# Kernel tuning notes

Measured on AMD Instinct MI355X. Metric: run time of the kernel, lower is better.

## Reference

```python
import jax, jax.numpy as jnp
import numpy as np

B, N, C = 4, 8192, 256
H, L = 8, 64
HD = C // H            # head_dim = 32
NB = N // L            # num_blocks = 128
EG_HID = 16            # EDGE_GATE_HIDDEN_DIM


def setup_inputs() -> dict:
    key = jax.random.key(0)
    ks = jax.random.split(key, 10)
    x = jax.random.normal(ks[0], (B, N, C), dtype=jnp.float32)
    attn_mask = (jax.random.uniform(ks[1], (B, NB, L, L)) < 0.3).astype(jnp.float32)
    edge_feats = jax.random.normal(ks[2], (B, NB, L, L, 4), dtype=jnp.float32)
    # parameters
    qkv_w = jax.random.normal(ks[3], (3 * C, C), dtype=jnp.float32) * (C ** -0.5)
    qkv_b = jnp.zeros((3 * C,), dtype=jnp.float32)
    proj_w = jax.random.normal(ks[4], (C, C), dtype=jnp.float32) * (C ** -0.5)
    proj_b = jnp.zeros((C,), dtype=jnp.float32)
    eg_w1 = jax.random.normal(ks[5], (EG_HID, 4), dtype=jnp.float32) * 0.01
    eg_b1 = jnp.zeros((EG_HID,), dtype=jnp.float32)
    eg_w2 = jax.random.normal(ks[6], (H, EG_HID), dtype=jnp.float32) * 0.01
    eg_b2 = jnp.zeros((H,), dtype=jnp.float32)
    return {"x": x, "attn_mask": attn_mask, "edge_feats": edge_feats,
            "qkv_w": qkv_w, "qkv_b": qkv_b, "proj_w": proj_w, "proj_b": proj_b,
            "eg_w1": eg_w1, "eg_b1": eg_b1, "eg_w2": eg_w2, "eg_b2": eg_b2}


def reference(x, attn_mask, edge_feats, qkv_w, qkv_b, proj_w, proj_b,
              eg_w1, eg_b1, eg_w2, eg_b2):
    scale = HD ** -0.5
    xb = x.reshape(B, NB, L, C)                      # (B, nb, L, C)
    eye = jnp.eye(L, dtype=x.dtype)                  # (L, L)

    # ensure every query row attends to >= 1 key: OR-in diagonal where row empty
    need_diag = (attn_mask.sum(-1) < 1).astype(x.dtype)          # (B, nb, L)
    diag_cur = jnp.diagonal(attn_mask, axis1=-2, axis2=-1)       # (B, nb, L)
    new_diag = jnp.maximum(diag_cur, need_diag)
    mask = attn_mask * (1.0 - eye) + new_diag[..., :, None] * eye  # (B, nb, L, L)

    # physics bias: zero the diagonal, set channel 3 to 1 on the diagonal
    diag_vec = jnp.array([0.0, 0.0, 0.0, 1.0], dtype=x.dtype)
    bp = jnp.where(eye[None, None, :, :, None] > 0, diag_vec, edge_feats)  # (B,nb,L,L,4)

    qkv = xb @ qkv_w.T + qkv_b                       # (B, nb, L, 3C)
    q = qkv[..., :C].reshape(B, NB, L, H, HD)
    k = qkv[..., C:2 * C].reshape(B, NB, L, H, HD)
    v = qkv[..., 2 * C:].reshape(B, NB, L, H, HD)

    scores = jnp.einsum('bnqhd,bnkhd->bnqkh', q, k) * scale + bp[..., 3:4]
    minf = jnp.array(-jnp.inf, dtype=scores.dtype)
    scores = jnp.where(mask[..., None] == 0, minf, scores)
    probs = jax.nn.softmax(scores, axis=3)           # softmax over key dim

    # per-head edge gate: Linear(4->16) -> GELU(exact) -> Linear(16->H)
    g = jax.nn.gelu(bp @ eg_w1.T + eg_b1, approximate=False) @ eg_w2.T + eg_b2
    g = jnp.where(mask[..., None] == 0, 0.0, g)      # (B, nb, L, L, H)

    xm = jnp.einsum('bnqkh,bnkhd->bnqhd', probs + g, v)  # (B, nb, L, H, HD)
    out = xm.reshape(B, NB, L, C) @ proj_w.T + proj_b
    return out.reshape(B, N, C)
```

## Files before the change

kernel.cpp:

```cpp
#include <hip/hip_runtime.h>
#include <math.h>

typedef unsigned short u16;
typedef unsigned long long u64;
typedef __attribute__((ext_vector_type(8))) short bf16x8;
typedef __attribute__((ext_vector_type(4))) float f32x4;
typedef __attribute__((ext_vector_type(2))) float v2f;

__device__ __forceinline__ float b2f(u16 u) {
  unsigned int i = ((unsigned int)u) << 16;
  return __builtin_bit_cast(float, i);
}
__device__ __forceinline__ u16 f2b(float f) {
  unsigned int x = __builtin_bit_cast(unsigned int, f);
  x += 0x7fffu + ((x >> 16) & 1u);
  return (u16)(x >> 16);
}

__device__ __forceinline__ v2f gelu2(v2f x) {
  v2f x2 = x * x;
  v2f p = x2 * 0.0099735626f + (-0.0664903813f);
  p = x2 * p + 0.3989422804f;
  v2f phi = x * p + 0.5f;
  return x * phi;
}

__device__ __forceinline__ void gload16(void* lds, const void* g) {
  __builtin_amdgcn_global_load_lds(
      (const __attribute__((address_space(1))) void*)g,
      (__attribute__((address_space(3))) void*)lds, 16, 0, 0);
}

template <bool OUT_F32, int KC>
__global__ __launch_bounds__(256) void gemm_bt16(
    const u16* __restrict__ A, const u16* __restrict__ W,
    const float* __restrict__ bias, void* __restrict__ outp,
    int M, int N) {
  __shared__ __align__(16) u16 As[2][128 * 32];
  __shared__ __align__(16) u16 Bs[2][128 * 32];
  const int tid = threadIdx.x;
  const int m0 = blockIdx.x * 128, n0 = blockIdx.y * 128;
  const int w = tid >> 6, lane = tid & 63;
  const int quad = lane >> 4, l16 = lane & 15;
  const int mw = (w >> 1) * 64, nw = (w & 1) * 64;
  const int r0 = tid >> 2, s0 = (tid & 3) * 8;
  const u16* a0 = A + (size_t)(m0 + r0) * KC + s0;
  const u16* a1 = A + (size_t)(m0 + 64 + r0) * KC + s0;
  const u16* b0 = W + (size_t)(n0 + r0) * KC + s0;
  const u16* b1 = W + (size_t)(n0 + 64 + r0) * KC + s0;

  f32x4 acc[4][4];
#pragma unroll
  for (int i = 0; i < 4; i++)
#pragma unroll
    for (int j = 0; j < 4; j++) acc[i][j] = (f32x4){0.f, 0.f, 0.f, 0.f};

  gload16(&As[0][tid * 8], a0);
  gload16(&As[0][(tid + 256) * 8], a1);
  gload16(&Bs[0][tid * 8], b0);
  gload16(&Bs[0][(tid + 256) * 8], b1);

  const int NT = KC >> 5;
#pragma unroll 2
  for (int t = 0; t < NT; ++t) {
    const int cur = t & 1;
    __syncthreads();
    bf16x8 af[4], bfr[4];
#pragma unroll
    for (int tt = 0; tt < 4; tt++) {
      af[tt] = ((const bf16x8*)As[cur])[(mw + 16 * tt + l16) * 4 + quad];
      bfr[tt] = ((const bf16x8*)Bs[cur])[(nw + 16 * tt + l16) * 4 + quad];
    }
    if (t + 1 < NT) {
      const int ko = (t + 1) * 32;
      gload16(&As[cur ^ 1][tid * 8], a0 + ko);
      gload16(&As[cur ^ 1][(tid + 256) * 8], a1 + ko);
      gload16(&Bs[cur ^ 1][tid * 8], b0 + ko);
      gload16(&Bs[cur ^ 1][(tid + 256) * 8], b1 + ko);
    }
#pragma unroll
    for (int ti = 0; ti < 4; ti++)
#pragma unroll
      for (int tj = 0; tj < 4; tj++)
        acc[ti][tj] = __builtin_amdgcn_mfma_f32_16x16x32_bf16(
            af[ti], bfr[tj], acc[ti][tj], 0, 0, 0);
  }

#pragma unroll
  for (int ti = 0; ti < 4; ti++) {
    int row = m0 + mw + 16 * ti + quad * 4;
#pragma unroll
    for (int tj = 0; tj < 4; tj++) {
      int col = n0 + nw + 16 * tj + l16;
      float bc = bias[col];
#pragma unroll
      for (int r = 0; r < 4; r++) {
        float v = acc[ti][tj][r] + bc;
        if (OUT_F32)
          ((float*)outp)[(size_t)(row + r) * N + col] = v;
        else
          ((u16*)outp)[(size_t)(row + r) * N + col] = f2b(v);
      }
    }
  }
}

__global__ __launch_bounds__(256) void gate_kernel(
    const float* __restrict__ mask, const float* __restrict__ edge,
    const float* __restrict__ w1, const float* __restrict__ b1,
    const float* __restrict__ w2, const float* __restrict__ b2,
    u16* __restrict__ g, u16* __restrict__ e3w, u64* __restrict__ mbw,
    const float* __restrict__ x, u16* __restrict__ xb,
    const float* __restrict__ qw, u16* __restrict__ qwb,
    const float* __restrict__ pw, u16* __restrict__ pwb) {
  const int blk = blockIdx.x >> 3, oct = blockIdx.x & 7, tid = threadIdx.x;
  const int gtid = blockIdx.x * 256 + tid;

  float4 cx0 = ((const float4*)x)[gtid];
  float4 cx1 = ((const float4*)x)[gtid + 1048576];
  float4 cw;
  ushort4* wdst = nullptr;
  int wj = 0;
  if (gtid < 49152) {
    wj = gtid; wdst = (ushort4*)qwb; cw = ((const float4*)qw)[wj];
  } else if (gtid < 65536) {
    wj = gtid - 49152; wdst = (ushort4*)pwb; cw = ((const float4*)pw)[wj];
  }

  __shared__ __align__(16) float W2s[128];
  __shared__ u64 mbits[8];
  if (tid < 128) W2s[tid] = w2[tid];
  if (tid < 32) {
    int q = tid >> 2, jp = tid & 3;
    int row = oct * 8 + q;
    const float* mr = mask + ((size_t)blk * 64 + row) * 64 + jp * 16;
    u64 bits = 0;
#pragma unroll
    for (int j = 0; j < 16; j++)
      if (mr[j] != 0.0f) bits |= 1ull << (jp * 16 + j);
    bits |= __shfl_xor(bits, 1);
    bits |= __shfl_xor(bits, 2);
    if (bits == 0ull) bits = 1ull << row;
    if (jp == 0) {
      mbits[q] = bits;
      mbw[(size_t)blk * 64 + row] = bits;
    }
  }
  __syncthreads();

  const int p0 = oct * 512 + tid, p1 = p0 + 256;
  const int qa = p0 >> 6, ka = p0 & 63;
  const int qb = p1 >> 6, kb = p1 & 63;
  float a0, a1, a2, a3, c0, c1, c2, c3;
  if (qa == ka) {
    a0 = a1 = a2 = 0.f; a3 = 1.f;
  } else {
    float4 e = *(const float4*)(edge + ((size_t)blk * 4096 + p0) * 4);
    a0 = e.x; a1 = e.y; a2 = e.z; a3 = e.w;
  }
  if (qb == kb) {
    c0 = c1 = c2 = 0.f; c3 = 1.f;
  } else {
    float4 e = *(const float4*)(edge + ((size_t)blk * 4096 + p1) * 4);
    c0 = e.x; c1 = e.y; c2 = e.z; c3 = e.w;
  }
  e3w[(size_t)blk * 4096 + p0] = f2b(a3);
  e3w[(size_t)blk * 4096 + p1] = f2b(c3);
  const bool ona = (mbits[qa & 7] >> ka) & 1ull;
  const bool onb = (mbits[qb & 7] >> kb) & 1ull;

  const v2f e0 = {a0, c0}, e1 = {a1, c1}, e2 = {a2, c2}, e3v = {a3, c3};
  v2f hd[16];
#pragma unroll
  for (int t = 0; t < 16; t++) {
    v2f h = e0 * w1[t * 4];
    h += e1 * w1[t * 4 + 1];
    h += e2 * w1[t * 4 + 2];
    h += e3v * w1[t * 4 + 3];
    h += b1[t];
    hd[t] = gelu2(h);
  }
  u16* gp = g + (size_t)blk * 32768;
#pragma unroll
  for (int hh = 0; hh < 8; hh++) {
    const f32x4 wa = *(const f32x4*)&W2s[hh * 16];
    const f32x4 wb = *(const f32x4*)&W2s[hh * 16 + 4];
    const f32x4 wc = *(const f32x4*)&W2s[hh * 16 + 8];
    const f32x4 wd = *(const f32x4*)&W2s[hh * 16 + 12];
    v2f s = hd[0] * wa.x;
    s += hd[1] * wa.y;  s += hd[2] * wa.z;  s += hd[3] * wa.w;
    s += hd[4] * wb.x;  s += hd[5] * wb.y;  s += hd[6] * wb.z;
    s += hd[7] * wb.w;  s += hd[8] * wc.x;  s += hd[9] * wc.y;
    s += hd[10] * wc.z; s += hd[11] * wc.w; s += hd[12] * wd.x;
    s += hd[13] * wd.y; s += hd[14] * wd.z; s += hd[15] * wd.w;
    float bb = b2[hh];
    gp[hh * 4096 + p0] = ona ? f2b(s.x + bb) : (u16)0;
    gp[hh * 4096 + p1] = onb ? f2b(s.y + bb) : (u16)0;
  }

  {
    ushort4 o;
    o.x = f2b(cx0.x); o.y = f2b(cx0.y); o.z = f2b(cx0.z); o.w = f2b(cx0.w);
    ((ushort4*)xb)[gtid] = o;
    o.x = f2b(cx1.x); o.y = f2b(cx1.y); o.z = f2b(cx1.z); o.w = f2b(cx1.w);
    ((ushort4*)xb)[gtid + 1048576] = o;
    if (wdst) {
      o.x = f2b(cw.x); o.y = f2b(cw.y); o.z = f2b(cw.z); o.w = f2b(cw.w);
      wdst[wj] = o;
    }
  }
}

__global__ __launch_bounds__(256) void attn_mfma(
    const u16* __restrict__ qkv, const u16* __restrict__ g,
    const u16* __restrict__ e3w, const u64* __restrict__ mbw,
    u16* __restrict__ xm) {
  __shared__ __align__(16) u16 qh[64 * 40];
  __shared__ __align__(16) u16 kh[64 * 40];
  __shared__ __align__(16) u16 vt[32 * 72];
  __shared__ __align__(16) u16 Pp[64 * 72];
  const int blk = blockIdx.x, h = blockIdx.y, tid = threadIdx.x;
  const int w = tid >> 6, lane = tid & 63;
  const int l16 = lane & 15, quad = lane >> 4;

  {
    int r = tid >> 2, d8 = (tid & 3) * 8;
    size_t base = ((size_t)(blk * 64 + r)) * 768 + h * 32 + d8;
    *(int4*)&qh[r * 40 + d8] = *(const int4*)(qkv + base);
    *(int4*)&kh[r * 40 + d8] = *(const int4*)(qkv + base + 256);
    u16 vv[8];
    *(int4*)vv = *(const int4*)(qkv + base + 512);
#pragma unroll
    for (int i = 0; i < 8; i++) vt[(d8 + i) * 72 + r] = vv[i];
  }
  const int q = w * 16 + l16;
  const u64 bq = mbw[(size_t)blk * 64 + q];
  __syncthreads();

  const float scale = 0.17677669529663687f;

  bf16x8 qf = *(const bf16x8*)&qh[q * 40 + quad * 8];
  f32x4 st[4];
  __builtin_amdgcn_s_setprio(1);
#pragma unroll
  for (int mt = 0; mt < 4; mt++) {
    bf16x8 kf = *(const bf16x8*)&kh[(mt * 16 + l16) * 40 + quad * 8];
    st[mt] = __builtin_amdgcn_mfma_f32_16x16x32_bf16(
        kf, qf, (f32x4){0.f, 0.f, 0.f, 0.f}, 0, 0, 0);
  }
  __builtin_amdgcn_s_setprio(0);
  const u16* e3q = e3w + (size_t)blk * 4096 + q * 64;
  const u16* gq  = g + ((size_t)(blk * 8 + h)) * 4096 + q * 64;
  float sv[4][4], mx = -1e30f;
#pragma unroll
  for (int mt = 0; mt < 4; mt++) {
    u16 e4[4];
    *(u64*)e4 = *(const u64*)(e3q + mt * 16 + quad * 4);
#pragma unroll
    for (int r = 0; r < 4; r++) {
      int key = mt * 16 + quad * 4 + r;
      float s = st[mt][r] * scale + b2f(e4[r]);
      bool on = (bq >> key) & 1ull;
      sv[mt][r] = on ? s : -1e30f;
      mx = fmaxf(mx, sv[mt][r]);
    }
  }
  mx = fmaxf(mx, __shfl_xor(mx, 16));
  mx = fmaxf(mx, __shfl_xor(mx, 32));
  float sum = 0.f;
#pragma unroll
  for (int mt = 0; mt < 4; mt++)
#pragma unroll
    for (int r = 0; r < 4; r++) {
      float e = __expf(sv[mt][r] - mx);
      sv[mt][r] = e;
      sum += e;
    }
  sum += __shfl_xor(sum, 16);
  sum += __shfl_xor(sum, 32);
  float inv = 1.0f / sum;

#pragma unroll
  for (int mt = 0; mt < 4; mt++) {
    u16 g4[4], o[4];
    *(u64*)g4 = *(const u64*)(gq + mt * 16 + quad * 4);
#pragma unroll
    for (int r = 0; r < 4; r++) o[r] = f2b(sv[mt][r] * inv + b2f(g4[r]));
    *(u64*)&Pp[q * 72 + mt * 16 + quad * 4] = *(u64*)o;
  }
  __builtin_amdgcn_s_waitcnt(0);

  f32x4 dm[2] = {(f32x4){0.f, 0.f, 0.f, 0.f}, (f32x4){0.f, 0.f, 0.f, 0.f}};
  __builtin_amdgcn_s_setprio(1);
#pragma unroll
  for (int kt = 0; kt < 2; kt++) {
    bf16x8 pf = *(const bf16x8*)&Pp[q * 72 + kt * 32 + quad * 8];
#pragma unroll
    for (int nt = 0; nt < 2; nt++) {
      bf16x8 vf = *(const bf16x8*)&vt[(nt * 16 + l16) * 72 + kt * 32 + quad * 8];
      dm[nt] = __builtin_amdgcn_mfma_f32_16x16x32_bf16(pf, vf, dm[nt], 0, 0, 0);
    }
  }
  __builtin_amdgcn_s_setprio(0);
#pragma unroll
  for (int nt = 0; nt < 2; nt++)
#pragma unroll
    for (int r = 0; r < 4; r++)
      qh[(w * 16 + quad * 4 + r) * 40 + nt * 16 + l16] = f2b(dm[nt][r]);
  __syncthreads();
  {
    int r = tid >> 2, d8 = (tid & 3) * 8;
    *(int4*)(xm + ((size_t)(blk * 64 + r)) * 256 + h * 32 + d8) =
        *(int4*)&qh[r * 40 + d8];
  }
}

extern "C" void kernel_launch(void* const* d_in, const int* in_sizes, int n_in,
                              void* d_out, int out_size, void* d_ws,
                              size_t ws_size, hipStream_t stream) {
  static const int RS[11] = {8388608, 2097152, 8388608, 196608, 768,
                             65536,   256,     64,      16,     128, 8};
  const float* P[11];
  for (int i = 0; i < 11; i++) P[i] = (const float*)d_in[i < n_in ? i : 0];
  bool dict_ok = (n_in >= 11);
  if (dict_ok)
    for (int i = 0; i < 11; i++)
      if (in_sizes[i] != RS[i]) { dict_ok = false; break; }
  if (!dict_ok) {
    bool seen84 = false;
    for (int i = 0; i < n_in && i < 16; i++) {
      int s = in_sizes[i], role = -1;
      if (s == 8388608) { role = seen84 ? 2 : 0; seen84 = true; }
      else
        for (int r = 1; r < 11; r++)
          if (r != 2 && RS[r] == s) { role = r; break; }
      if (role >= 0 && role < 11) P[role] = (const float*)d_in[i];
    }
  }
  float* out = (float*)d_out;
  char* ws = (char*)d_ws;
  u16* qkv = (u16*)ws;
  u16* g   = (u16*)(ws + 50331648);
  u16* e3w = (u16*)(ws + 83886080);
  u64* mbw = (u64*)(ws + 88080384);
  u16* xmb = (u16*)(ws + 88342528);
  u16* pwb = (u16*)(ws + 105119744);
  u16* qwb = (u16*)(ws + 105250816);
  u16* xb = xmb;

  gate_kernel<<<4096, 256, 0, stream>>>(P[1], P[2], P[7], P[8], P[9], P[10],
                                        g, e3w, mbw, P[0], xb, P[3], qwb,
                                        P[5], pwb);
  gemm_bt16<false, 256><<<dim3(256, 6), 256, 0, stream>>>(
      xb, qwb, P[4], qkv, 32768, 768);
  attn_mfma<<<dim3(512, 8), 256, 0, stream>>>(qkv, g, e3w, mbw, xmb);
  gemm_bt16<true, 256><<<dim3(256, 2), 256, 0, stream>>>(
      xmb, pwb, P[6], out, 32768, 256);
}
```

Before: 200.9 us.

## Fuse attention over all heads with output projection in one kernel

Each block now loops over all 8 heads for its 64-token window and keeps the per-head attention outputs in shared memory. It then multiplies that 64x256 tile by the projection weight with MFMA and writes the fp32 output directly, with Q/K/V for the next head prefetched into registers during the loop. This removes the xm round-trip through global memory and one kernel launch. In exchange the grid drops from 4096 to 512 blocks, shared memory use per block grows, and the projection weight is streamed from global memory by every block.

```diff
diff --git a/kernel.cpp b/kernel.cpp
--- a/kernel.cpp
+++ b/kernel.cpp
@@ -211,107 +211,152 @@
   }
 }
 
-__global__ __launch_bounds__(256) void attn_mfma(
+__global__ __launch_bounds__(256) void attn_proj(
     const u16* __restrict__ qkv, const u16* __restrict__ g,
     const u16* __restrict__ e3w, const u64* __restrict__ mbw,
-    u16* __restrict__ xm) {
+    const u16* __restrict__ pwb, const float* __restrict__ pb,
+    float* __restrict__ out) {
   __shared__ __align__(16) u16 qh[64 * 40];
   __shared__ __align__(16) u16 kh[64 * 40];
   __shared__ __align__(16) u16 vt[32 * 72];
   __shared__ __align__(16) u16 Pp[64 * 72];
-  const int blk = blockIdx.x, h = blockIdx.y, tid = threadIdx.x;
+  __shared__ __align__(16) u16 xms[64 * 264];
+  const int blk = blockIdx.x, tid = threadIdx.x;
   const int w = tid >> 6, lane = tid & 63;
   const int l16 = lane & 15, quad = lane >> 4;
-
-  {
-    int r = tid >> 2, d8 = (tid & 3) * 8;
-    size_t base = ((size_t)(blk * 64 + r)) * 768 + h * 32 + d8;
-    *(int4*)&qh[r * 40 + d8] = *(const int4*)(qkv + base);
-    *(int4*)&kh[r * 40 + d8] = *(const int4*)(qkv + base + 256);
-    u16 vv[8];
-    *(int4*)vv = *(const int4*)(qkv + base + 512);
-#pragma unroll
-    for (int i = 0; i < 8; i++) vt[(d8 + i) * 72 + r] = vv[i];
-  }
+  const int r = tid >> 2, d8 = (tid & 3) * 8;
+  const size_t base = ((size_t)(blk * 64 + r)) * 768 + d8;
   const int q = w * 16 + l16;
   const u64 bq = mbw[(size_t)blk * 64 + q];
-  __syncthreads();
-
   const float scale = 0.17677669529663687f;
 
-  bf16x8 qf = *(const bf16x8*)&qh[q * 40 + quad * 8];
-  f32x4 st[4];
-  __builtin_amdgcn_s_setprio(1);
+  int4 pq = *(const int4*)(qkv + base);
+  int4 pk = *(const int4*)(qkv + base + 256);
+  int4 pv = *(const int4*)(qkv + base + 512);
+
+#pragma unroll 1
+  for (int h = 0; h < 8; ++h) {
+    *(int4*)&qh[r * 40 + d8] = pq;
+    *(int4*)&kh[r * 40 + d8] = pk;
+    u16 vv[8];
+    *(int4*)vv = pv;
+#pragma unroll
+    for (int i = 0; i < 8; i++) vt[(d8 + i) * 72 + r] = vv[i];
+    if (h < 7) {
+      pq = *(const int4*)(qkv + base + (h + 1) * 32);
+      pk = *(const int4*)(qkv + base + (h + 1) * 32 + 256);
+      pv = *(const int4*)(qkv + base + (h + 1) * 32 + 512);
+    }
+    __syncthreads();
+
+    bf16x8 qf = *(const bf16x8*)&qh[q * 40 + quad * 8];
+    f32x4 st[4];
+    __builtin_amdgcn_s_setprio(1);
+#pragma unroll
+    for (int mt = 0; mt < 4; mt++) {
+      bf16x8 kf = *(const bf16x8*)&kh[(mt * 16 + l16) * 40 + quad * 8];
+      st[mt] = __builtin_amdgcn_mfma_f32_16x16x32_bf16(
+          kf, qf, (f32x4){0.f, 0.f, 0.f, 0.f}, 0, 0, 0);
+    }
+    __builtin_amdgcn_s_setprio(0);
+    const u16* e3q = e3w + (size_t)blk * 4096 + q * 64;
+    const u16* gq = g + ((size_t)(blk * 8 + h)) * 4096 + q * 64;
+    float sv[4][4], mx = -1e30f;
+#pragma unroll
+    for (int mt = 0; mt < 4; mt++) {
+      u16 e4[4];
+      *(u64*)e4 = *(const u64*)(e3q + mt * 16 + quad * 4);
+#pragma unroll
+      for (int rr = 0; rr < 4; rr++) {
+        int key = mt * 16 + quad * 4 + rr;
+        float s = st[mt][rr] * scale + b2f(e4[rr]);
+        bool on = (bq >> key) & 1ull;
+        sv[mt][rr] = on ? s : -1e30f;
+        mx = fmaxf(mx, sv[mt][rr]);
+      }
+    }
+    mx = fmaxf(mx, __shfl_xor(mx, 16));
+    mx = fmaxf(mx, __shfl_xor(mx, 32));
+    float sum = 0.f;
+#pragma unroll
+    for (int mt = 0; mt < 4; mt++)
+#pragma unroll
+      for (int rr = 0; rr < 4; rr++) {
+        float e = __expf(sv[mt][rr] - mx);
+        sv[mt][rr] = e;
+        sum += e;
+      }
+    sum += __shfl_xor(sum, 16);
+    sum += __shfl_xor(sum, 32);
+    float inv = 1.0f / sum;
+
+#pragma unroll
+    for (int mt = 0; mt < 4; mt++) {
+      u16 g4[4], o[4];
+      *(u64*)g4 = *(const u64*)(gq + mt * 16 + quad * 4);
+#pragma unroll
+      for (int rr = 0; rr < 4; rr++)
+        o[rr] = f2b(sv[mt][rr] * inv + b2f(g4[rr]));
+      *(u64*)&Pp[q * 72 + mt * 16 + quad * 4] = *(u64*)o;
+    }
+    __builtin_amdgcn_s_waitcnt(0);
+
+    f32x4 dm[2] = {(f32x4){0.f, 0.f, 0.f, 0.f}, (f32x4){0.f, 0.f, 0.f, 0.f}};
+    __builtin_amdgcn_s_setprio(1);
+#pragma unroll
+    for (int kt = 0; kt < 2; kt++) {
+      bf16x8 pf = *(const bf16x8*)&Pp[q * 72 + kt * 32 + quad * 8];
+#pragma unroll
+      for (int nt = 0; nt < 2; nt++) {
+        bf16x8 vf =
+            *(const bf16x8*)&vt[(nt * 16 + l16) * 72 + kt * 32 + quad * 8];
+        dm[nt] =
+            __builtin_amdgcn_mfma_f32_16x16x32_bf16(pf, vf, dm[nt], 0, 0, 0);
+      }
+    }
+    __builtin_amdgcn_s_setprio(0);
+#pragma unroll
+    for (int nt = 0; nt < 2; nt++)
+#pragma unroll
+      for (int rr = 0; rr < 4; rr++)
+        xms[(w * 16 + quad * 4 + rr) * 264 + h * 32 + nt * 16 + l16] =
+            f2b(dm[nt][rr]);
+    __syncthreads();
+  }
+
+  f32x4 acc[4][4];
+#pragma unroll
+  for (int i = 0; i < 4; i++)
+#pragma unroll
+    for (int j = 0; j < 4; j++) acc[i][j] = (f32x4){0.f, 0.f, 0.f, 0.f};
+#pragma unroll
+  for (int k0 = 0; k0 < 256; k0 += 32) {
+    bf16x8 af[4], bfr[4];
+#pragma unroll
+    for (int mt = 0; mt < 4; mt++)
+      af[mt] = *(const bf16x8*)&xms[(mt * 16 + l16) * 264 + k0 + quad * 8];
+#pragma unroll
+    for (int tj = 0; tj < 4; tj++)
+      bfr[tj] = *(const bf16x8*)(pwb + (size_t)(w * 64 + tj * 16 + l16) * 256 +
+                                 k0 + quad * 8);
+#pragma unroll
+    for (int mt = 0; mt < 4; mt++)
+#pragma unroll
+      for (int tj = 0; tj < 4; tj++)
+        acc[mt][tj] = __builtin_amdgcn_mfma_f32_16x16x32_bf16(
+            af[mt], bfr[tj], acc[mt][tj], 0, 0, 0);
+  }
 #pragma unroll
   for (int mt = 0; mt < 4; mt++) {
-    bf16x8 kf = *(const bf16x8*)&kh[(mt * 16 + l16) * 40 + quad * 8];
-    st[mt] = __builtin_amdgcn_mfma_f32_16x16x32_bf16(
-        kf, qf, (f32x4){0.f, 0.f, 0.f, 0.f}, 0, 0, 0);
-  }
-  __builtin_amdgcn_s_setprio(0);
-  const u16* e3q = e3w + (size_t)blk * 4096 + q * 64;
-  const u16* gq  = g + ((size_t)(blk * 8 + h)) * 4096 + q * 64;
-  float sv[4][4], mx = -1e30f;
-#pragma unroll
-  for (int mt = 0; mt < 4; mt++) {
-    u16 e4[4];
-    *(u64*)e4 = *(const u64*)(e3q + mt * 16 + quad * 4);
-#pragma unroll
-    for (int r = 0; r < 4; r++) {
-      int key = mt * 16 + quad * 4 + r;
-      float s = st[mt][r] * scale + b2f(e4[r]);
-      bool on = (bq >> key) & 1ull;
-      sv[mt][r] = on ? s : -1e30f;
-      mx = fmaxf(mx, sv[mt][r]);
-    }
-  }
-  mx = fmaxf(mx, __shfl_xor(mx, 16));
-  mx = fmaxf(mx, __shfl_xor(mx, 32));
-  float sum = 0.f;
-#pragma unroll
-  for (int mt = 0; mt < 4; mt++)
-#pragma unroll
-    for (int r = 0; r < 4; r++) {
-      float e = __expf(sv[mt][r] - mx);
-      sv[mt][r] = e;
-      sum += e;
-    }
-  sum += __shfl_xor(sum, 16);
-  sum += __shfl_xor(sum, 32);
-  float inv = 1.0f / sum;
-
-#pragma unroll
-  for (int mt = 0; mt < 4; mt++) {
-    u16 g4[4], o[4];
-    *(u64*)g4 = *(const u64*)(gq + mt * 16 + quad * 4);
-#pragma unroll
-    for (int r = 0; r < 4; r++) o[r] = f2b(sv[mt][r] * inv + b2f(g4[r]));
-    *(u64*)&Pp[q * 72 + mt * 16 + quad * 4] = *(u64*)o;
-  }
-  __builtin_amdgcn_s_waitcnt(0);
-
-  f32x4 dm[2] = {(f32x4){0.f, 0.f, 0.f, 0.f}, (f32x4){0.f, 0.f, 0.f, 0.f}};
-  __builtin_amdgcn_s_setprio(1);
-#pragma unroll
-  for (int kt = 0; kt < 2; kt++) {
-    bf16x8 pf = *(const bf16x8*)&Pp[q * 72 + kt * 32 + quad * 8];
-#pragma unroll
-    for (int nt = 0; nt < 2; nt++) {
-      bf16x8 vf = *(const bf16x8*)&vt[(nt * 16 + l16) * 72 + kt * 32 + quad * 8];
-      dm[nt] = __builtin_amdgcn_mfma_f32_16x16x32_bf16(pf, vf, dm[nt], 0, 0, 0);
-    }
-  }
-  __builtin_amdgcn_s_setprio(0);
-#pragma unroll
-  for (int nt = 0; nt < 2; nt++)
-#pragma unroll
-    for (int r = 0; r < 4; r++)
-      qh[(w * 16 + quad * 4 + r) * 40 + nt * 16 + l16] = f2b(dm[nt][r]);
-  __syncthreads();
-  {
-    int r = tid >> 2, d8 = (tid & 3) * 8;
-    *(int4*)(xm + ((size_t)(blk * 64 + r)) * 256 + h * 32 + d8) =
-        *(int4*)&qh[r * 40 + d8];
+    int row = blk * 64 + mt * 16 + quad * 4;
+#pragma unroll
+    for (int tj = 0; tj < 4; tj++) {
+      int col = w * 64 + tj * 16 + l16;
+      float bc = pb[col];
+#pragma unroll
+      for (int rr = 0; rr < 4; rr++)
+        out[(size_t)(row + rr) * 256 + col] = acc[mt][tj][rr] + bc;
+    }
   }
 }
 
@@ -343,17 +388,14 @@
   u16* g   = (u16*)(ws + 50331648);
   u16* e3w = (u16*)(ws + 83886080);
   u64* mbw = (u64*)(ws + 88080384);
-  u16* xmb = (u16*)(ws + 88342528);
+  u16* xb  = (u16*)(ws + 88342528);
   u16* pwb = (u16*)(ws + 105119744);
   u16* qwb = (u16*)(ws + 105250816);
-  u16* xb = xmb;
 
   gate_kernel<<<4096, 256, 0, stream>>>(P[1], P[2], P[7], P[8], P[9], P[10],
                                         g, e3w, mbw, P[0], xb, P[3], qwb,
                                         P[5], pwb);
   gemm_bt16<false, 256><<<dim3(256, 6), 256, 0, stream>>>(
       xb, qwb, P[4], qkv, 32768, 768);
-  attn_mfma<<<dim3(512, 8), 256, 0, stream>>>(qkv, g, e3w, mbw, xmb);
-  gemm_bt16<true, 256><<<dim3(256, 2), 256, 0, stream>>>(
-      xmb, pwb, P[6], out, 32768, 256);
-}
+  attn_proj<<<512, 256, 0, stream>>>(qkv, g, e3w, mbw, pwb, P[6], out);
+}
```

New measurement: 192.1 us (median of 2 runs). 1.05x faster.
